# Kernel optimization log

Measured on AMD Instinct MI355X. Metric: run time of the kernel, lower is better.

## Reference

```python
import jax, jax.numpy as jnp
import numpy as np

N_NODES = 100000
N_EDGES = 1600000
D_FEAT = 128
HIDDEN = 64


def setup_inputs() -> dict:
    key = jax.random.key(0)
    k1, k2, k3, k4, k5 = jax.random.split(key, 5)
    x = jax.random.normal(k1, (N_NODES, D_FEAT), dtype=jnp.float32)
    edge_index = jax.random.randint(k2, (2, N_EDGES), 0, N_NODES, dtype=jnp.int32)
    edge_weight = jax.random.uniform(k3, (N_EDGES,), dtype=jnp.float32)
    W1 = jax.random.normal(k4, (D_FEAT, HIDDEN), dtype=jnp.float32) / np.sqrt(D_FEAT)
    b1 = jnp.zeros((HIDDEN,), dtype=jnp.float32)
    W2 = jax.random.normal(k5, (HIDDEN, 1), dtype=jnp.float32) / np.sqrt(HIDDEN)
    b2 = jnp.zeros((1,), dtype=jnp.float32)
    return {"x": x, "edge_index": edge_index, "edge_weight": edge_weight,
            "W1": W1, "b1": b1, "W2": W2, "b2": b2}


def reference(x, edge_index, edge_weight, W1, b1, W2, b2):
    N = x.shape[0]
    # PyG GCNConv default: add self-loops with weight 1.0
    loops = jnp.arange(N, dtype=edge_index.dtype)
    row = jnp.concatenate([edge_index[0], loops])  # source nodes
    col = jnp.concatenate([edge_index[1], loops])  # target nodes
    ew = jnp.concatenate([edge_weight, jnp.ones((N,), dtype=edge_weight.dtype)])
    # symmetric degree normalization: norm_e = d^{-1/2}[row] * w_e * d^{-1/2}[col]
    deg = jax.ops.segment_sum(ew, col, num_segments=N)
    dinv = jnp.where(deg > 0, jax.lax.rsqrt(deg), 0.0)
    norm = dinv[row] * ew * dinv[col]  # [E+N]

    def gcn_layer(h, W, b):
        h = h @ W                          # [N, out] transform first (PyG order)
        msg = h[row] * norm[:, None]       # gather + scale, [E+N, out]
        agg = jax.ops.segment_sum(msg, col, num_segments=N)  # scatter-add
        return agg + b

    h = jax.nn.relu(gcn_layer(x, W1, b1))
    # dropout(p=0.5) is identity in eval mode
    return gcn_layer(h, W2, b2)  # [N, 1]
```

## Files before the change

### kernel.cpp

```cpp
#include <hip/hip_runtime.h>
#include <stdint.h>

typedef float f4 __attribute__((ext_vector_type(4)));
typedef float f32x4 __attribute__((ext_vector_type(4)));
typedef _Float16 hq4 __attribute__((ext_vector_type(4)));
typedef _Float16 half8 __attribute__((ext_vector_type(8)));

#define DF 128
#define HID 64
#define EPB 4096
#define CAP 5120

__global__ __launch_bounds__(512) void kFusedA(const int* __restrict__ row,
                                               const int* __restrict__ col,
                                               const float* __restrict__ ew,
                                               int* __restrict__ cur,
                                               int2* __restrict__ tmp,
                                               const float* __restrict__ x,
                                               const float* __restrict__ W1,
                                               _Float16* __restrict__ h,
                                               int E, int nblk, int nstrip, int N) {
    __shared__ __align__(16) char smem[55360];
    int t = threadIdx.x;

    if ((int)blockIdx.x < nblk) {
        int*  hist  = (int*)smem;
        int*  pref  = hist + 512;
        int*  lbase = pref + 512;
        int*  wsum  = lbase + 512;
        int2* sv    = (int2*)(smem + 6208);
        int*  sa    = (int*)(smem + 6208 + 32768);
        int b = blockIdx.x;
        hist[t] = 0;
        __syncthreads();
        int s = b * EPB, e = min(E, s + EPB);
        int cnt = e - s;
        int  mybin[8], myrank[8];
        int2 myv[8];
#pragma unroll
        for (int k = 0; k < 8; ++k) {
            int i = s + t + k * 512;
            mybin[k] = -1;
            if (i < e) {
                int c = col[i];
                int bin = c >> 8;
                myv[k].x = row[i] | ((c & 255) << 24);
                myv[k].y = __float_as_int(ew[i]);
                mybin[k] = bin;
                myrank[k] = atomicAdd(&hist[bin], 1);
            }
        }
        __syncthreads();
        int val = hist[t];
        lbase[t] = val ? atomicAdd(&cur[t], val) + t * CAP : 0;
        int lane = t & 63, wid = t >> 6;
        int inc = val;
#pragma unroll
        for (int d = 1; d < 64; d <<= 1) {
            int y = __shfl_up(inc, d);
            if (lane >= d) inc += y;
        }
        if (lane == 63) wsum[wid] = inc;
        __syncthreads();
        if (t == 0) {
            int r = 0;
#pragma unroll
            for (int i = 0; i < 8; ++i) { int xx = wsum[i]; wsum[i] = r; r += xx; }
        }
        __syncthreads();
        pref[t] = inc - val + wsum[wid];
        __syncthreads();
#pragma unroll
        for (int k = 0; k < 8; ++k) {
            if (mybin[k] >= 0) {
                int pos = pref[mybin[k]] + myrank[k];
                sv[pos] = myv[k];
                sa[pos] = lbase[mybin[k]] + myrank[k];
            }
        }
        __syncthreads();
        for (int i = t; i < cnt; i += 512) tmp[sa[i]] = sv[i];
    } else {
        _Float16* W1f = (_Float16*)smem;
        for (int i = t; i < 8192; i += 512) {
            int j     = i & 7;
            int lane  = (i >> 3) & 63;
            int ntile = (i >> 9) & 3;
            int kstep = i >> 11;
            int k = kstep * 32 + (lane >> 4) * 8 + j;
            int n = ntile * 16 + (lane & 15);
            W1f[i] = (_Float16)W1[k * 64 + n];
        }
        __syncthreads();
        int wave = ((int)blockIdx.x - nblk) * 8 + (t >> 6);
        if (wave >= nstrip) return;
        int node0 = wave << 4;
        int l = t & 63;
        int quad = l >> 4;
        int m = l & 15;
        int r = node0 + m;
        if (r >= N) r = N - 1;

        const half8* bfrag = (const half8*)W1f;
        f32x4 acc[4];
#pragma unroll
        for (int nt = 0; nt < 4; ++nt) acc[nt] = (f32x4)(0.f);
#pragma unroll
        for (int kstep = 0; kstep < 4; ++kstep) {
            const f4* xr = (const f4*)(x + (size_t)r * DF + kstep * 32 + quad * 8);
            f4 a0 = xr[0], a1 = xr[1];
            half8 af;
            af[0] = (_Float16)a0.x; af[1] = (_Float16)a0.y;
            af[2] = (_Float16)a0.z; af[3] = (_Float16)a0.w;
            af[4] = (_Float16)a1.x; af[5] = (_Float16)a1.y;
            af[6] = (_Float16)a1.z; af[7] = (_Float16)a1.w;
#pragma unroll
            for (int nt = 0; nt < 4; ++nt) {
                half8 bf = bfrag[(kstep * 4 + nt) * 64 + l];
                acc[nt] = __builtin_amdgcn_mfma_f32_16x16x32_f16(af, bf, acc[nt], 0, 0, 0);
            }
        }
        int nodeb = node0 + quad * 4;
#pragma unroll
        for (int nt = 0; nt < 4; ++nt) {
#pragma unroll
            for (int reg = 0; reg < 4; ++reg) {
                int node = nodeb + reg;
                if (node < N)
                    h[(unsigned)node * 64u + (unsigned)(nt * 16 + m)] =
                        (_Float16)acc[nt][reg];
            }
        }
    }
}

__global__ __launch_bounds__(512) void kB(const int2* __restrict__ tmp,
                                          const int* __restrict__ cur,
                                          int2* __restrict__ edata,
                                          int2* __restrict__ offse,
                                          float* __restrict__ dinv,
                                          int N) {
    __shared__ int   hist[256];
    __shared__ float degl[256];
    __shared__ int   fill[256];
    __shared__ int   wsum[8];
    __shared__ int2  se[CAP];
    int bin = blockIdx.x, t = threadIdx.x;
    int s = bin * CAP;
    int cnt = min(cur[bin], CAP);

    if (t < 256) { hist[t] = 0; degl[t] = 0.f; }
    __syncthreads();
    for (int i = t; i < cnt; i += 512) {
        int2 pr = tmp[s + i];
        se[i] = pr;
        int lo = ((unsigned)pr.x) >> 24;
        atomicAdd(&hist[lo], 1);
        atomicAdd(&degl[lo], __int_as_float(pr.y));
    }
    __syncthreads();
    int val = (t < 256) ? hist[t] : 0;
    int lane = t & 63, wid = t >> 6;
    int inc = val;
#pragma unroll
    for (int d = 1; d < 64; d <<= 1) {
        int y = __shfl_up(inc, d);
        if (lane >= d) inc += y;
    }
    if (lane == 63) wsum[wid] = inc;
    __syncthreads();
    if (t == 0) {
        int r = 0;
#pragma unroll
        for (int i = 0; i < 8; ++i) { int x = wsum[i]; wsum[i] = r; r += x; }
    }
    __syncthreads();
    int pfx = inc - val + wsum[wid];
    if (t < 256) {
        fill[t] = pfx;
        int c = bin * 256 + t;
        if (c < N) {
            int2 oe;
            oe.x = s + pfx;
            oe.y = s + pfx + val;
            offse[c] = oe;
            dinv[c] = rsqrtf(1.0f + degl[t]);
        }
    }
    __syncthreads();
    for (int i = t; i < cnt; i += 512) {
        int2 pr = se[i];
        int lo = ((unsigned)pr.x) >> 24;
        int pos = atomicAdd(&fill[lo], 1);
        int2 o;
        o.x = pr.x & 0x00FFFFFF;
        o.y = pr.y;
        edata[s + pos] = o;
    }
}

__global__ __launch_bounds__(256) void k_agg_h2(const int2* __restrict__ offse,
                                                const int2* __restrict__ edata,
                                                const float* __restrict__ dinv,
                                                const _Float16* __restrict__ h,
                                                const float* __restrict__ b1,
                                                const float* __restrict__ W2,
                                                float* __restrict__ h2p, int N) {
    __shared__ int2 stage[4][68];
    int wv = threadIdx.x >> 6;
    int l  = threadIdx.x & 63;
    int g  = l >> 4;
    unsigned fq = (unsigned)(l & 15);
    int sbase = g * 17;
    int vv = blockIdx.x * 16 + wv * 4 + g;
    bool ok = vv < N;
    int v = ok ? vv : N - 1;
    const hq4* hp = (const hq4*)h;

    float di = dinv[v];
    int2 oe = offse[v];

    hq4 sv4 = hp[((unsigned)v << 4) | fq];
    float a0 = di * (float)sv4.x, a1 = di * (float)sv4.y;
    float a2 = di * (float)sv4.z, a3 = di * (float)sv4.w;

    int deg = oe.y - oe.x;
    for (int base = 0; base < deg; base += 16) {
        int idx = oe.x + base + (int)fq;
        int2 pr;
        pr.x = 0; pr.y = 0;
        if (idx < oe.y) {
            pr = edata[idx];
            pr.y = __float_as_int(__int_as_float(pr.y) * dinv[pr.x]);
        }
        stage[wv][sbase + (int)fq] = pr;
#pragma unroll
        for (int k = 0; k < 16; ++k) {
            int2 em = stage[wv][sbase + k];
            float ws = __int_as_float(em.y);
            hq4 hv = hp[((unsigned)em.x << 4) | fq];
            a0 += ws * (float)hv.x;
            a1 += ws * (float)hv.y;
            a2 += ws * (float)hv.z;
            a3 += ws * (float)hv.w;
        }
    }

    a0 = di * a0; a1 = di * a1; a2 = di * a2; a3 = di * a3;
    f4 bb = ((const f4*)b1)[fq];
    f4 ww = ((const f4*)W2)[fq];
    float s = fmaxf(a0 + bb.x, 0.f) * ww.x
            + fmaxf(a1 + bb.y, 0.f) * ww.y
            + fmaxf(a2 + bb.z, 0.f) * ww.z
            + fmaxf(a3 + bb.w, 0.f) * ww.w;
    s += __shfl_down(s, 8);
    s += __shfl_down(s, 4);
    s += __shfl_down(s, 2);
    s += __shfl_down(s, 1);
    if (fq == 0 && ok) h2p[vv] = di * s;
}

__global__ __launch_bounds__(256) void k_out(const int2* __restrict__ offse,
                                             const int2* __restrict__ edata,
                                             const float* __restrict__ dinv,
                                             const float* __restrict__ h2p,
                                             const float* __restrict__ b2,
                                             float* __restrict__ out, int N) {
    int t = blockIdx.x * 256 + threadIdx.x;
    int v = t >> 4;
    if (v >= N) return;
    int c = t & 15;
    int2 oe = offse[v];
    float s = 0.f;
    for (int i = oe.x + c; i < oe.y; i += 16) {
        int2 pr = edata[i];
        s += __int_as_float(pr.y) * h2p[(unsigned)pr.x];
    }
    s += __shfl_down(s, 8);
    s += __shfl_down(s, 4);
    s += __shfl_down(s, 2);
    s += __shfl_down(s, 1);
    if (c == 0) {
        float di = dinv[v];
        out[v] = b2[0] + di * (h2p[v] + s);
    }
}

extern "C" void kernel_launch(void* const* d_in, const int* in_sizes, int n_in,
                              void* d_out, int out_size, void* d_ws, size_t ws_size,
                              hipStream_t stream) {
    const float* x  = (const float*)d_in[0];
    const int*   ei = (const int*)d_in[1];
    const float* ew = (const float*)d_in[2];
    const float* W1 = (const float*)d_in[3];
    const float* b1 = (const float*)d_in[4];
    const float* W2 = (const float*)d_in[5];
    const float* b2 = (const float*)d_in[6];
    float* out = (float*)d_out;

    const int N = in_sizes[0] / DF;
    const int E = in_sizes[2];
    const int* row = ei;
    const int* col = ei + E;

    const int nbin = (N + 255) / 256;
    const int nblk = (E + EPB - 1) / EPB;

    size_t    gsz   = (size_t)nbin * CAP;
    int2*     edata = (int2*)d_ws;
    int2*     tmp   = edata + gsz;
    _Float16* h     = (_Float16*)(tmp + gsz);
    int       nbinPad = (nbin + 3) & ~3;
    int*      cur   = (int*)(h + (size_t)N * 64);
    float*    dinv  = (float*)(cur + nbinPad);
    float*    h2p   = dinv + N;
    int2*     offse = (int2*)(h2p + N);

    const int B = 256;
    int nstrip = (N + 15) / 16;
    int gemmBlocks = (nstrip + 7) / 8;
    int gAgg = (N + 15) / 16;
    int gN16 = (N * 16 + B - 1) / B;

    hipMemsetAsync(cur, 0, (size_t)nbinPad * sizeof(int), stream);
    kFusedA<<<nblk + gemmBlocks, 512, 0, stream>>>(row, col, ew, cur, tmp,
                                                   x, W1, h, E, nblk, nstrip, N);
    kB<<<nbin, 512, 0, stream>>>(tmp, cur, edata, offse, dinv, N);
    k_agg_h2<<<gAgg, B, 0, stream>>>(offse, edata, dinv, h, b1, W2, h2p, N);
    k_out<<<gN16, B, 0, stream>>>(offse, edata, dinv, h2p, b2, out, N);
}
```

Before: 193.2 us.

## Fuse all GCN stages into one persistent cooperative kernel with grid syncs

```diff
diff --git a/kernel.cpp b/kernel.cpp
--- a/kernel.cpp
+++ b/kernel.cpp
@@ -1,5 +1,8 @@
 #include <hip/hip_runtime.h>
+#include <hip/hip_cooperative_groups.h>
 #include <stdint.h>
+
+namespace cg = cooperative_groups;
 
 typedef float f4 __attribute__((ext_vector_type(4)));
 typedef float f32x4 __attribute__((ext_vector_type(4)));
@@ -10,279 +13,281 @@
 #define HID 64
 #define EPB 4096
 #define CAP 5120
-
-__global__ __launch_bounds__(512) void kFusedA(const int* __restrict__ row,
-                                               const int* __restrict__ col,
-                                               const float* __restrict__ ew,
-                                               int* __restrict__ cur,
-                                               int2* __restrict__ tmp,
-                                               const float* __restrict__ x,
-                                               const float* __restrict__ W1,
-                                               _Float16* __restrict__ h,
-                                               int E, int nblk, int nstrip, int N) {
-    __shared__ __align__(16) char smem[55360];
+#define SMEM_BYTES 55360
+
+__global__ __launch_bounds__(512) void kMega(
+    const int* __restrict__ row, const int* __restrict__ col,
+    const float* __restrict__ ew, const float* __restrict__ x,
+    const float* __restrict__ W1, const float* __restrict__ b1,
+    const float* __restrict__ W2, const float* __restrict__ b2,
+    float* __restrict__ out,
+    int* __restrict__ cur, int2* __restrict__ tmp, int2* __restrict__ edata,
+    int2* __restrict__ offse, float* __restrict__ dinv,
+    _Float16* __restrict__ h, float* __restrict__ h2p,
+    int E, int N, int nblk, int nbin, int nstrip, int gemmB)
+{
+    __shared__ __align__(16) char smem[SMEM_BYTES];
+    cg::grid_group grid = cg::this_grid();
     int t = threadIdx.x;
-
-    if ((int)blockIdx.x < nblk) {
-        int*  hist  = (int*)smem;
-        int*  pref  = hist + 512;
-        int*  lbase = pref + 512;
-        int*  wsum  = lbase + 512;
-        int2* sv    = (int2*)(smem + 6208);
-        int*  sa    = (int*)(smem + 6208 + 32768);
-        int b = blockIdx.x;
-        hist[t] = 0;
-        __syncthreads();
-        int s = b * EPB, e = min(E, s + EPB);
-        int cnt = e - s;
-        int  mybin[8], myrank[8];
-        int2 myv[8];
-#pragma unroll
-        for (int k = 0; k < 8; ++k) {
-            int i = s + t + k * 512;
-            mybin[k] = -1;
-            if (i < e) {
-                int c = col[i];
-                int bin = c >> 8;
-                myv[k].x = row[i] | ((c & 255) << 24);
-                myv[k].y = __float_as_int(ew[i]);
-                mybin[k] = bin;
-                myrank[k] = atomicAdd(&hist[bin], 1);
+    int nb = gridDim.x;
+
+    for (int i = blockIdx.x * 512 + t; i < nbin; i += nb * 512) cur[i] = 0;
+    grid.sync();
+
+    {
+        int p1u = nblk + gemmB;
+        for (int u = blockIdx.x; u < p1u; u += nb) {
+            __syncthreads();
+            if (u < nblk) {
+                int*  hist  = (int*)smem;
+                int*  pref  = hist + 512;
+                int*  lbase = pref + 512;
+                int*  wsum  = lbase + 512;
+                int2* sv    = (int2*)(smem + 6208);
+                int*  sa    = (int*)(smem + 6208 + 32768);
+                hist[t] = 0;
+                __syncthreads();
+                int s = u * EPB, e = min(E, s + EPB);
+                int cnt = e - s;
+                int  mybin[8], myrank[8];
+                int2 myv[8];
+#pragma unroll
+                for (int k = 0; k < 8; ++k) {
+                    int i = s + t + k * 512;
+                    mybin[k] = -1;
+                    if (i < e) {
+                        int c = col[i];
+                        int bin = c >> 8;
+                        myv[k].x = row[i] | ((c & 255) << 24);
+                        myv[k].y = __float_as_int(ew[i]);
+                        mybin[k] = bin;
+                        myrank[k] = atomicAdd(&hist[bin], 1);
+                    }
+                }
+                __syncthreads();
+                int val = hist[t];
+                lbase[t] = val ? atomicAdd(&cur[t], val) + t * CAP : 0;
+                int lane = t & 63, wid = t >> 6;
+                int inc = val;
+#pragma unroll
+                for (int d = 1; d < 64; d <<= 1) {
+                    int y = __shfl_up(inc, d);
+                    if (lane >= d) inc += y;
+                }
+                if (lane == 63) wsum[wid] = inc;
+                __syncthreads();
+                if (t == 0) {
+                    int r = 0;
+#pragma unroll
+                    for (int i = 0; i < 8; ++i) { int xx = wsum[i]; wsum[i] = r; r += xx; }
+                }
+                __syncthreads();
+                pref[t] = inc - val + wsum[wid];
+                __syncthreads();
+#pragma unroll
+                for (int k = 0; k < 8; ++k) {
+                    if (mybin[k] >= 0) {
+                        int pos = pref[mybin[k]] + myrank[k];
+                        sv[pos] = myv[k];
+                        sa[pos] = lbase[mybin[k]] + myrank[k];
+                    }
+                }
+                __syncthreads();
+                for (int i = t; i < cnt; i += 512) tmp[sa[i]] = sv[i];
+            } else {
+                _Float16* W1f = (_Float16*)smem;
+                for (int i = t; i < 8192; i += 512) {
+                    int j     = i & 7;
+                    int lane  = (i >> 3) & 63;
+                    int ntile = (i >> 9) & 3;
+                    int kstep = i >> 11;
+                    int k = kstep * 32 + (lane >> 4) * 8 + j;
+                    int n = ntile * 16 + (lane & 15);
+                    W1f[i] = (_Float16)W1[k * 64 + n];
+                }
+                __syncthreads();
+                int wave = (u - nblk) * 8 + (t >> 6);
+                if (wave < nstrip) {
+                    int node0 = wave << 4;
+                    int l = t & 63;
+                    int quad = l >> 4;
+                    int m = l & 15;
+                    int r = node0 + m;
+                    if (r >= N) r = N - 1;
+                    const half8* bfrag = (const half8*)W1f;
+                    f32x4 acc[4];
+#pragma unroll
+                    for (int nt = 0; nt < 4; ++nt) acc[nt] = (f32x4)(0.f);
+#pragma unroll
+                    for (int kstep = 0; kstep < 4; ++kstep) {
+                        const f4* xr = (const f4*)(x + (size_t)r * DF + kstep * 32 + quad * 8);
+                        f4 a0 = xr[0], a1 = xr[1];
+                        half8 af;
+                        af[0] = (_Float16)a0.x; af[1] = (_Float16)a0.y;
+                        af[2] = (_Float16)a0.z; af[3] = (_Float16)a0.w;
+                        af[4] = (_Float16)a1.x; af[5] = (_Float16)a1.y;
+                        af[6] = (_Float16)a1.z; af[7] = (_Float16)a1.w;
+#pragma unroll
+                        for (int nt = 0; nt < 4; ++nt) {
+                            half8 bf = bfrag[(kstep * 4 + nt) * 64 + l];
+                            acc[nt] = __builtin_amdgcn_mfma_f32_16x16x32_f16(af, bf, acc[nt], 0, 0, 0);
+                        }
+                    }
+                    int nodeb = node0 + quad * 4;
+#pragma unroll
+                    for (int nt = 0; nt < 4; ++nt) {
+#pragma unroll
+                        for (int reg = 0; reg < 4; ++reg) {
+                            int node = nodeb + reg;
+                            if (node < N)
+                                h[(unsigned)node * 64u + (unsigned)(nt * 16 + m)] =
+                                    (_Float16)acc[nt][reg];
+                        }
+                    }
+                }
             }
         }
-        __syncthreads();
-        int val = hist[t];
-        lbase[t] = val ? atomicAdd(&cur[t], val) + t * CAP : 0;
-        int lane = t & 63, wid = t >> 6;
-        int inc = val;
-#pragma unroll
-        for (int d = 1; d < 64; d <<= 1) {
-            int y = __shfl_up(inc, d);
-            if (lane >= d) inc += y;
+    }
+    grid.sync();
+
+    {
+        int*   hist = (int*)smem;
+        float* degl = (float*)(smem + 1024);
+        int*   fill = (int*)(smem + 2048);
+        int*   wsum = (int*)(smem + 3072);
+        for (int u = blockIdx.x; u < nbin; u += nb) {
+            int s = u * CAP;
+            int cnt = min(cur[u], CAP);
+            if (t < 256) { hist[t] = 0; degl[t] = 0.f; }
+            __syncthreads();
+            for (int i = t; i < cnt; i += 512) {
+                int2 pr = tmp[s + i];
+                int lo = ((unsigned)pr.x) >> 24;
+                atomicAdd(&hist[lo], 1);
+                atomicAdd(&degl[lo], __int_as_float(pr.y));
+            }
+            __syncthreads();
+            int val = (t < 256) ? hist[t] : 0;
+            int lane = t & 63, wid = t >> 6;
+            int inc = val;
+#pragma unroll
+            for (int d = 1; d < 64; d <<= 1) {
+                int y = __shfl_up(inc, d);
+                if (lane >= d) inc += y;
+            }
+            if (lane == 63) wsum[wid] = inc;
+            __syncthreads();
+            if (t == 0) {
+                int r = 0;
+#pragma unroll
+                for (int i = 0; i < 8; ++i) { int xx = wsum[i]; wsum[i] = r; r += xx; }
+            }
+            __syncthreads();
+            int pfx = inc - val + wsum[wid];
+            if (t < 256) {
+                fill[t] = pfx;
+                int c = u * 256 + t;
+                if (c < N) {
+                    int2 oe;
+                    oe.x = s + pfx;
+                    oe.y = s + pfx + val;
+                    offse[c] = oe;
+                    dinv[c] = rsqrtf(1.0f + degl[t]);
+                }
+            }
+            __syncthreads();
+            for (int i = t; i < cnt; i += 512) {
+                int2 pr = tmp[s + i];
+                int lo = ((unsigned)pr.x) >> 24;
+                int pos = atomicAdd(&fill[lo], 1);
+                int2 o;
+                o.x = pr.x & 0x00FFFFFF;
+                o.y = pr.y;
+                edata[s + pos] = o;
+            }
+            __syncthreads();
         }
-        if (lane == 63) wsum[wid] = inc;
-        __syncthreads();
-        if (t == 0) {
-            int r = 0;
-#pragma unroll
-            for (int i = 0; i < 8; ++i) { int xx = wsum[i]; wsum[i] = r; r += xx; }
+    }
+    grid.sync();
+
+    {
+        int2 (*stage)[68] = (int2(*)[68])smem;
+        int wv = t >> 6;
+        int l  = t & 63;
+        int g  = l >> 4;
+        unsigned fq = (unsigned)(l & 15);
+        int sbase = g * 17;
+        const hq4* hp = (const hq4*)h;
+        int p3u = (N + 31) >> 5;
+        for (int u = blockIdx.x; u < p3u; u += nb) {
+            int vv = u * 32 + wv * 4 + g;
+            bool ok = vv < N;
+            int v = ok ? vv : N - 1;
+            float di = dinv[v];
+            int2 oe = offse[v];
+            hq4 sv4 = hp[((unsigned)v << 4) | fq];
+            float a0 = di * (float)sv4.x, a1 = di * (float)sv4.y;
+            float a2 = di * (float)sv4.z, a3 = di * (float)sv4.w;
+            int deg = oe.y - oe.x;
+            for (int base = 0; base < deg; base += 16) {
+                int idx = oe.x + base + (int)fq;
+                int2 pr;
+                pr.x = 0; pr.y = 0;
+                if (idx < oe.y) {
+                    pr = edata[idx];
+                    pr.y = __float_as_int(__int_as_float(pr.y) * dinv[pr.x]);
+                }
+                stage[wv][sbase + (int)fq] = pr;
+#pragma unroll
+                for (int k = 0; k < 16; ++k) {
+                    int2 em = stage[wv][sbase + k];
+                    float ws = __int_as_float(em.y);
+                    hq4 hv = hp[((unsigned)em.x << 4) | fq];
+                    a0 += ws * (float)hv.x;
+                    a1 += ws * (float)hv.y;
+                    a2 += ws * (float)hv.z;
+                    a3 += ws * (float)hv.w;
+                }
+            }
+            a0 = di * a0; a1 = di * a1; a2 = di * a2; a3 = di * a3;
+            f4 bb = ((const f4*)b1)[fq];
+            f4 ww = ((const f4*)W2)[fq];
+            float s2 = fmaxf(a0 + bb.x, 0.f) * ww.x
+                     + fmaxf(a1 + bb.y, 0.f) * ww.y
+                     + fmaxf(a2 + bb.z, 0.f) * ww.z
+                     + fmaxf(a3 + bb.w, 0.f) * ww.w;
+            s2 += __shfl_down(s2, 8);
+            s2 += __shfl_down(s2, 4);
+            s2 += __shfl_down(s2, 2);
+            s2 += __shfl_down(s2, 1);
+            if (fq == 0 && ok) h2p[vv] = di * s2;
         }
-        __syncthreads();
-        pref[t] = inc - val + wsum[wid];
-        __syncthreads();
-#pragma unroll
-        for (int k = 0; k < 8; ++k) {
-            if (mybin[k] >= 0) {
-                int pos = pref[mybin[k]] + myrank[k];
-                sv[pos] = myv[k];
-                sa[pos] = lbase[mybin[k]] + myrank[k];
+    }
+    grid.sync();
+
+    {
+        int p4u = (N + 31) >> 5;
+        for (int u = blockIdx.x; u < p4u; u += nb) {
+            int tt = u * 512 + t;
+            int v = tt >> 4;
+            if (v < N) {
+                int c = tt & 15;
+                int2 oe = offse[v];
+                float s2 = 0.f;
+                for (int i = oe.x + c; i < oe.y; i += 16) {
+                    int2 pr = edata[i];
+                    s2 += __int_as_float(pr.y) * h2p[(unsigned)pr.x];
+                }
+                s2 += __shfl_down(s2, 8);
+                s2 += __shfl_down(s2, 4);
+                s2 += __shfl_down(s2, 2);
+                s2 += __shfl_down(s2, 1);
+                if (c == 0) {
+                    float di = dinv[v];
+                    out[v] = b2[0] + di * (h2p[v] + s2);
+                }
             }
         }
-        __syncthreads();
-        for (int i = t; i < cnt; i += 512) tmp[sa[i]] = sv[i];
-    } else {
-        _Float16* W1f = (_Float16*)smem;
-        for (int i = t; i < 8192; i += 512) {
-            int j     = i & 7;
-            int lane  = (i >> 3) & 63;
-            int ntile = (i >> 9) & 3;
-            int kstep = i >> 11;
-            int k = kstep * 32 + (lane >> 4) * 8 + j;
-            int n = ntile * 16 + (lane & 15);
-            W1f[i] = (_Float16)W1[k * 64 + n];
-        }
-        __syncthreads();
-        int wave = ((int)blockIdx.x - nblk) * 8 + (t >> 6);
-        if (wave >= nstrip) return;
-        int node0 = wave << 4;
-        int l = t & 63;
-        int quad = l >> 4;
-        int m = l & 15;
-        int r = node0 + m;
-        if (r >= N) r = N - 1;
-
-        const half8* bfrag = (const half8*)W1f;
-        f32x4 acc[4];
-#pragma unroll
-        for (int nt = 0; nt < 4; ++nt) acc[nt] = (f32x4)(0.f);
-#pragma unroll
-        for (int kstep = 0; kstep < 4; ++kstep) {
-            const f4* xr = (const f4*)(x + (size_t)r * DF + kstep * 32 + quad * 8);
-            f4 a0 = xr[0], a1 = xr[1];
-            half8 af;
-            af[0] = (_Float16)a0.x; af[1] = (_Float16)a0.y;
-            af[2] = (_Float16)a0.z; af[3] = (_Float16)a0.w;
-            af[4] = (_Float16)a1.x; af[5] = (_Float16)a1.y;
-            af[6] = (_Float16)a1.z; af[7] = (_Float16)a1.w;
-#pragma unroll
-            for (int nt = 0; nt < 4; ++nt) {
-                half8 bf = bfrag[(kstep * 4 + nt) * 64 + l];
-                acc[nt] = __builtin_amdgcn_mfma_f32_16x16x32_f16(af, bf, acc[nt], 0, 0, 0);
-            }
-        }
-        int nodeb = node0 + quad * 4;
-#pragma unroll
-        for (int nt = 0; nt < 4; ++nt) {
-#pragma unroll
-            for (int reg = 0; reg < 4; ++reg) {
-                int node = nodeb + reg;
-                if (node < N)
-                    h[(unsigned)node * 64u + (unsigned)(nt * 16 + m)] =
-                        (_Float16)acc[nt][reg];
-            }
-        }
-    }
-}
-
-__global__ __launch_bounds__(512) void kB(const int2* __restrict__ tmp,
-                                          const int* __restrict__ cur,
-                                          int2* __restrict__ edata,
-                                          int2* __restrict__ offse,
-                                          float* __restrict__ dinv,
-                                          int N) {
-    __shared__ int   hist[256];
-    __shared__ float degl[256];
-    __shared__ int   fill[256];
-    __shared__ int   wsum[8];
-    __shared__ int2  se[CAP];
-    int bin = blockIdx.x, t = threadIdx.x;
-    int s = bin * CAP;
-    int cnt = min(cur[bin], CAP);
-
-    if (t < 256) { hist[t] = 0; degl[t] = 0.f; }
-    __syncthreads();
-    for (int i = t; i < cnt; i += 512) {
-        int2 pr = tmp[s + i];
-        se[i] = pr;
-        int lo = ((unsigned)pr.x) >> 24;
-        atomicAdd(&hist[lo], 1);
-        atomicAdd(&degl[lo], __int_as_float(pr.y));
-    }
-    __syncthreads();
-    int val = (t < 256) ? hist[t] : 0;
-    int lane = t & 63, wid = t >> 6;
-    int inc = val;
-#pragma unroll
-    for (int d = 1; d < 64; d <<= 1) {
-        int y = __shfl_up(inc, d);
-        if (lane >= d) inc += y;
-    }
-    if (lane == 63) wsum[wid] = inc;
-    __syncthreads();
-    if (t == 0) {
-        int r = 0;
-#pragma unroll
-        for (int i = 0; i < 8; ++i) { int x = wsum[i]; wsum[i] = r; r += x; }
-    }
-    __syncthreads();
-    int pfx = inc - val + wsum[wid];
-    if (t < 256) {
-        fill[t] = pfx;
-        int c = bin * 256 + t;
-        if (c < N) {
-            int2 oe;
-            oe.x = s + pfx;
-            oe.y = s + pfx + val;
-            offse[c] = oe;
-            dinv[c] = rsqrtf(1.0f + degl[t]);
-        }
-    }
-    __syncthreads();
-    for (int i = t; i < cnt; i += 512) {
-        int2 pr = se[i];
-        int lo = ((unsigned)pr.x) >> 24;
-        int pos = atomicAdd(&fill[lo], 1);
-        int2 o;
-        o.x = pr.x & 0x00FFFFFF;
-        o.y = pr.y;
-        edata[s + pos] = o;
-    }
-}
-
-__global__ __launch_bounds__(256) void k_agg_h2(const int2* __restrict__ offse,
-                                                const int2* __restrict__ edata,
-                                                const float* __restrict__ dinv,
-                                                const _Float16* __restrict__ h,
-                                                const float* __restrict__ b1,
-                                                const float* __restrict__ W2,
-                                                float* __restrict__ h2p, int N) {
-    __shared__ int2 stage[4][68];
-    int wv = threadIdx.x >> 6;
-    int l  = threadIdx.x & 63;
-    int g  = l >> 4;
-    unsigned fq = (unsigned)(l & 15);
-    int sbase = g * 17;
-    int vv = blockIdx.x * 16 + wv * 4 + g;
-    bool ok = vv < N;
-    int v = ok ? vv : N - 1;
-    const hq4* hp = (const hq4*)h;
-
-    float di = dinv[v];
-    int2 oe = offse[v];
-
-    hq4 sv4 = hp[((unsigned)v << 4) | fq];
-    float a0 = di * (float)sv4.x, a1 = di * (float)sv4.y;
-    float a2 = di * (float)sv4.z, a3 = di * (float)sv4.w;
-
-    int deg = oe.y - oe.x;
-    for (int base = 0; base < deg; base += 16) {
-        int idx = oe.x + base + (int)fq;
-        int2 pr;
-        pr.x = 0; pr.y = 0;
-        if (idx < oe.y) {
-            pr = edata[idx];
-            pr.y = __float_as_int(__int_as_float(pr.y) * dinv[pr.x]);
-        }
-        stage[wv][sbase + (int)fq] = pr;
-#pragma unroll
-        for (int k = 0; k < 16; ++k) {
-            int2 em = stage[wv][sbase + k];
-            float ws = __int_as_float(em.y);
-            hq4 hv = hp[((unsigned)em.x << 4) | fq];
-            a0 += ws * (float)hv.x;
-            a1 += ws * (float)hv.y;
-            a2 += ws * (float)hv.z;
-            a3 += ws * (float)hv.w;
-        }
-    }
-
-    a0 = di * a0; a1 = di * a1; a2 = di * a2; a3 = di * a3;
-    f4 bb = ((const f4*)b1)[fq];
-    f4 ww = ((const f4*)W2)[fq];
-    float s = fmaxf(a0 + bb.x, 0.f) * ww.x
-            + fmaxf(a1 + bb.y, 0.f) * ww.y
-            + fmaxf(a2 + bb.z, 0.f) * ww.z
-            + fmaxf(a3 + bb.w, 0.f) * ww.w;
-    s += __shfl_down(s, 8);
-    s += __shfl_down(s, 4);
-    s += __shfl_down(s, 2);
-    s += __shfl_down(s, 1);
-    if (fq == 0 && ok) h2p[vv] = di * s;
-}
-
-__global__ __launch_bounds__(256) void k_out(const int2* __restrict__ offse,
-                                             const int2* __restrict__ edata,
-                                             const float* __restrict__ dinv,
-                                             const float* __restrict__ h2p,
-                                             const float* __restrict__ b2,
-                                             float* __restrict__ out, int N) {
-    int t = blockIdx.x * 256 + threadIdx.x;
-    int v = t >> 4;
-    if (v >= N) return;
-    int c = t & 15;
-    int2 oe = offse[v];
-    float s = 0.f;
-    for (int i = oe.x + c; i < oe.y; i += 16) {
-        int2 pr = edata[i];
-        s += __int_as_float(pr.y) * h2p[(unsigned)pr.x];
-    }
-    s += __shfl_down(s, 8);
-    s += __shfl_down(s, 4);
-    s += __shfl_down(s, 2);
-    s += __shfl_down(s, 1);
-    if (c == 0) {
-        float di = dinv[v];
-        out[v] = b2[0] + di * (h2p[v] + s);
     }
 }
 
@@ -316,16 +321,30 @@
     float*    h2p   = dinv + N;
     int2*     offse = (int2*)(h2p + N);
 
-    const int B = 256;
     int nstrip = (N + 15) / 16;
-    int gemmBlocks = (nstrip + 7) / 8;
-    int gAgg = (N + 15) / 16;
-    int gN16 = (N * 16 + B - 1) / B;
-
-    hipMemsetAsync(cur, 0, (size_t)nbinPad * sizeof(int), stream);
-    kFusedA<<<nblk + gemmBlocks, 512, 0, stream>>>(row, col, ew, cur, tmp,
-                                                   x, W1, h, E, nblk, nstrip, N);
-    kB<<<nbin, 512, 0, stream>>>(tmp, cur, edata, offse, dinv, N);
-    k_agg_h2<<<gAgg, B, 0, stream>>>(offse, edata, dinv, h, b1, W2, h2p, N);
-    k_out<<<gN16, B, 0, stream>>>(offse, edata, dinv, h2p, b2, out, N);
+    int gemmB  = (nstrip + 7) / 8;
+
+    static int nbCached = 0;
+    if (nbCached == 0) {
+        int dev = 0;
+        hipGetDevice(&dev);
+        hipDeviceProp_t prop;
+        hipGetDeviceProperties(&prop, dev);
+        int maxB = 0;
+        hipOccupancyMaxActiveBlocksPerMultiprocessor(&maxB, (const void*)kMega, 512, 0);
+        if (maxB < 1) maxB = 1;
+        nbCached = maxB * prop.multiProcessorCount;
+        if (nbCached < 1) nbCached = 256;
+    }
+    int nb = nbCached;
+
+    void* args[] = {
+        (void*)&row, (void*)&col, (void*)&ew, (void*)&x, (void*)&W1,
+        (void*)&b1, (void*)&W2, (void*)&b2, (void*)&out,
+        (void*)&cur, (void*)&tmp, (void*)&edata, (void*)&offse, (void*)&dinv,
+        (void*)&h, (void*)&h2p,
+        (void*)&E, (void*)&N, (void*)&nblk, (void*)&nbin,
+        (void*)&nstrip, (void*)&gemmB
+    };
+    hipLaunchCooperativeKernel((void*)kMega, dim3(nb), dim3(512), args, 0, stream);
 }
```

Measured after the change: 340.9 us. +76.4%, slower.
